# Optimization experiments

Hardware: AMD Instinct MI355X
Metric: run time of the kernel (lower is better)

The kernel has to match this reference:

```python
import jax, jax.numpy as jnp
import numpy as np

C = 512
NUM_HEADS = 8
GROUPS = 32
EPS = 1e-5


def setup_inputs() -> dict:
    key = jax.random.key(0)
    ks = jax.random.split(key, 7)
    B, H, W = 8, 32, 32
    x = jax.random.normal(ks[0], (B, C, H, W), dtype=jnp.float32)
    gn_w = jnp.ones((C,), dtype=jnp.float32)
    gn_b = jnp.zeros((C,), dtype=jnp.float32)
    # 1x1 convs as dense matrices [out, in]
    qkv_w = jax.random.normal(ks[1], (3 * C, C), dtype=jnp.float32) * (1.0 / np.sqrt(C))
    qkv_b = jnp.zeros((3 * C,), dtype=jnp.float32)
    proj_w = jax.random.normal(ks[2], (C, C), dtype=jnp.float32) * (1.0 / np.sqrt(C))
    proj_b = jnp.zeros((C,), dtype=jnp.float32)
    return {"x": x, "gn_w": gn_w, "gn_b": gn_b, "qkv_w": qkv_w,
            "qkv_b": qkv_b, "proj_w": proj_w, "proj_b": proj_b}


def reference(x, gn_w, gn_b, qkv_w, qkv_b, proj_w, proj_b):
    B, Cc, H, W = x.shape
    nh = NUM_HEADS
    d = Cc // nh
    N = H * W

    # GroupNorm(32, C) with affine
    xg = x.reshape(B, GROUPS, Cc // GROUPS, H, W)
    mean = jnp.mean(xg, axis=(2, 3, 4), keepdims=True)
    var = jnp.var(xg, axis=(2, 3, 4), keepdims=True)
    hn = ((xg - mean) * jax.lax.rsqrt(var + EPS)).reshape(B, Cc, H, W)
    hn = hn * gn_w[None, :, None, None] + gn_b[None, :, None, None]

    # 1x1 conv QKV projection: [B, 3C, H, W]
    qkv = jnp.einsum('oc,bchw->bohw', qkv_w, hn) + qkv_b[None, :, None, None]
    q, k, v = jnp.split(qkv, 3, axis=1)

    def to_heads(t):  # [B, C, H, W] -> [B, nh, N, d]
        return t.reshape(B, nh, d, N).transpose(0, 1, 3, 2)

    q, k, v = to_heads(q), to_heads(k), to_heads(v)
    scale = d ** (-0.5)
    attn = jax.nn.softmax(jnp.einsum('bhnd,bhmd->bhnm', q, k) * scale, axis=-1)
    o = jnp.einsum('bhnm,bhmd->bhnd', attn, v)          # [B, nh, N, d]
    o = o.transpose(0, 1, 3, 2).reshape(B, Cc, H, W)

    # 1x1 conv output projection + residual
    o = jnp.einsum('oc,bchw->bohw', proj_w, o) + proj_b[None, :, None, None]
    return x + o
```

## Files before the change

### kernel.cpp

```cpp
#include <hip/hip_runtime.h>

typedef __bf16 bf16x8 __attribute__((ext_vector_type(8)));
typedef float f32x4 __attribute__((ext_vector_type(4)));

#define MFMA(a, b, c) __builtin_amdgcn_mfma_f32_16x16x32_bf16(a, b, c, 0, 0, 0)

#define CS 0.18033688011112042f

__device__ __forceinline__ ushort f2bf(float f) {
    __bf16 h = (__bf16)f;
    return *(ushort*)&h;
}

__device__ __forceinline__ void stage_tile64(ushort* lds, const ushort* gbase,
                                             int row_stride, int nchunks,
                                             int wave, int lane) {
    int r8 = lane >> 3;
    int cswz = ((lane & 7) ^ r8) << 4;
#pragma unroll
    for (int c = wave; c < nchunks; c += 4) {
        const char* g = (const char*)(gbase + (size_t)(c * 8 + r8) * row_stride) + cswz;
        __builtin_amdgcn_global_load_lds(
            (const __attribute__((address_space(1))) unsigned int*)g,
            (__attribute__((address_space(3))) unsigned int*)((char*)lds + c * 1024),
            16, 0, 0);
    }
}

__device__ __forceinline__ bf16x8 lds_read_row(const ushort* lds, int row, int cb) {
    return *(const bf16x8*)((const char*)lds + row * 128 + (cb ^ ((row & 7) << 4)));
}

__global__ __launch_bounds__(256) void gn_cvt_kernel(const float* __restrict__ x,
                                                     const float* __restrict__ gnw,
                                                     const float* __restrict__ gnb,
                                                     ushort* __restrict__ hnT,
                                                     const float* __restrict__ w1,
                                                     const float* __restrict__ w2,
                                                     ushort* __restrict__ o1,
                                                     ushort* __restrict__ o2) {
    if (blockIdx.x >= 256) {
        int t = (blockIdx.x - 256) * 256 + threadIdx.x;
        const int n1q = (1536 * 512) / 4;
        float4 v;
        ushort* dst;
        int idx;
        if (t < n1q) {
            v = ((const float4*)w1)[t]; dst = o1; idx = t;
        } else {
            idx = t - n1q;
            v = ((const float4*)w2)[idx]; dst = o2;
        }
        ushort4 p;
        p.x = f2bf(v.x); p.y = f2bf(v.y); p.z = f2bf(v.z); p.w = f2bf(v.w);
        ((ushort4*)dst)[idx] = p;
        return;
    }

    int b = blockIdx.x >> 5, g = blockIdx.x & 31;
    const float* xp = x + (size_t)(b * 512 + g * 16) * 1024;
    int t = threadIdx.x;

    float s = 0.f, ss = 0.f;
    const float4* xp4 = (const float4*)xp;
    for (int i = t; i < 4096; i += 256) {
        float4 v = xp4[i];
        s += (v.x + v.y) + (v.z + v.w);
        ss += (v.x * v.x + v.y * v.y) + (v.z * v.z + v.w * v.w);
    }
#pragma unroll
    for (int off = 32; off >= 1; off >>= 1) {
        s += __shfl_xor(s, off);
        ss += __shfl_xor(ss, off);
    }
    __shared__ float red[8];
    __shared__ float sw[16], sb[16];
    int wave = t >> 6;
    if ((t & 63) == 0) { red[wave] = s; red[wave + 4] = ss; }
    if (t < 16) { sw[t] = gnw[g * 16 + t]; sb[t] = gnb[g * 16 + t]; }
    __syncthreads();
    float S = red[0] + red[1] + red[2] + red[3];
    float SS = red[4] + red[5] + red[6] + red[7];
    float mean = S * (1.0f / 16384.0f);
    float var = SS * (1.0f / 16384.0f) - mean * mean;
    float rstd = rsqrtf(var + 1e-5f);

    __shared__ ushort tile[16][258];
    int cc0 = (t & 3) * 4;
    int nb = t >> 2;
    for (int chunk = 0; chunk < 4; ++chunk) {
        __syncthreads();
#pragma unroll
        for (int cc = 0; cc < 16; ++cc) {
            float v = xp[cc * 1024 + chunk * 256 + t];
            tile[cc][t] = f2bf((v - mean) * rstd * sw[cc] + sb[cc]);
        }
        __syncthreads();
        size_t rowbase = (size_t)b * 1024 + chunk * 256;
#pragma unroll
        for (int k = 0; k < 4; ++k) {
            int nl = nb + 64 * k;
            ushort4 p;
            p.x = tile[cc0 + 0][nl];
            p.y = tile[cc0 + 1][nl];
            p.z = tile[cc0 + 2][nl];
            p.w = tile[cc0 + 3][nl];
            *(ushort4*)(hnT + (rowbase + nl) * 512 + g * 16 + cc0) = p;
        }
    }
}

__global__ __launch_bounds__(256) void gemm_qkv(const ushort* __restrict__ Wb,
                                                const ushort* __restrict__ hnT,
                                                const float* __restrict__ qkvb,
                                                ushort* __restrict__ qT,
                                                ushort* __restrict__ kT,
                                                ushort* __restrict__ vb) {
    int lane = threadIdx.x & 63, wave = threadIdx.x >> 6;
    int l15 = lane & 15, lg = lane >> 4;
    int bi = blockIdx.x;
    int b = bi & 7;
    int slot = bi >> 3;
    int m0 = (slot % 12) * 128;
    int n0 = (slot / 12) * 128;
    int mw = (wave >> 1) * 64, nw = (wave & 1) * 64;
    const ushort* bb = hnT + (size_t)b * 524288;

    __shared__ ushort abuf[2][8192];
    __shared__ ushort bbuf[2][8192];

    f32x4 acc[4][4] = {};
    stage_tile64(abuf[0], Wb + (size_t)m0 * 512, 512, 16, wave, lane);
    stage_tile64(bbuf[0], bb + (size_t)n0 * 512, 512, 16, wave, lane);
    __syncthreads();
    int cur = 0;
#pragma unroll 1
    for (int t = 0; t < 8; ++t) {
        if (t < 7) {
            stage_tile64(abuf[cur ^ 1], Wb + (size_t)m0 * 512 + (t + 1) * 64, 512, 16, wave, lane);
            stage_tile64(bbuf[cur ^ 1], bb + (size_t)n0 * 512 + (t + 1) * 64, 512, 16, wave, lane);
        }
#pragma unroll
        for (int kh = 0; kh < 2; kh++) {
            bf16x8 af[4], bfr[4];
#pragma unroll
            for (int i = 0; i < 4; i++)
                af[i] = lds_read_row(abuf[cur], mw + i * 16 + l15, kh * 64 + lg * 16);
#pragma unroll
            for (int j = 0; j < 4; j++)
                bfr[j] = lds_read_row(bbuf[cur], nw + j * 16 + l15, kh * 64 + lg * 16);
#pragma unroll
            for (int i = 0; i < 4; i++)
#pragma unroll
                for (int j = 0; j < 4; j++)
                    acc[i][j] = MFMA(af[i], bfr[j], acc[i][j]);
        }
        __syncthreads();
        cur ^= 1;
    }

#pragma unroll
    for (int i = 0; i < 4; i++) {
        int ob = m0 + mw + i * 16 + lg * 4;
        float bias[4];
#pragma unroll
        for (int r = 0; r < 4; r++) bias[r] = qkvb[ob + r];
        int part = ob >> 9;
        int oo = ob & 511;
#pragma unroll
        for (int j = 0; j < 4; j++) {
            int n = n0 + nw + j * 16 + l15;
            if (part == 2) {
                int L = n & 63;
                int cf = L >> 4;
                int s = ((cf >> 1) << 5) | (((L >> 2) & 3) << 3) | ((cf & 1) << 2) | (L & 3);
                int np = (n & ~63) | s;
#pragma unroll
                for (int r = 0; r < 4; r++)
                    vb[(size_t)(b * 512 + oo + r) * 1024 + np] = f2bf(acc[i][j][r] + bias[r]);
            } else {
                ushort* dst = part ? kT : qT;
                float sc = part ? 1.0f : CS;
                int h = oo >> 6, dd = oo & 63;
                ushort4 p;
                p.x = f2bf((acc[i][j][0] + bias[0]) * sc);
                p.y = f2bf((acc[i][j][1] + bias[1]) * sc);
                p.z = f2bf((acc[i][j][2] + bias[2]) * sc);
                p.w = f2bf((acc[i][j][3] + bias[3]) * sc);
                *(ushort4*)(dst + ((size_t)((b * 8 + h) * 1024 + n)) * 64 + dd) = p;
            }
        }
    }
}

__global__ __launch_bounds__(256) void attn_kernel(const ushort* __restrict__ qT,
                                                   const ushort* __restrict__ kT,
                                                   const ushort* __restrict__ vb,
                                                   ushort* __restrict__ aoT) {
    int bi = blockIdx.x;
    int bh = ((bi >> 6) << 3) | (bi & 7);
    int q0 = ((bi >> 3) & 7) * 128;
    int b = bh >> 3, h = bh & 7;
    int lane = threadIdx.x & 63, wave = threadIdx.x >> 6;
    int l15 = lane & 15, lg = lane >> 4;
    const ushort* qp = qT + (size_t)bh * 65536;
    const ushort* kp = kT + (size_t)bh * 65536;
    const ushort* vp = vb + (size_t)bh * 65536;

    __shared__ ushort kbuf[3][4096];
    __shared__ ushort vbuf[3][4096];

    bf16x8 vone;
#pragma unroll
    for (int e = 0; e < 8; e++) vone[e] = (__bf16)1.0f;

    bf16x8 qf[2][2];
#pragma unroll
    for (int i = 0; i < 2; i++)
#pragma unroll
        for (int kh = 0; kh < 2; kh++)
            qf[i][kh] = *(const bf16x8*)(qp + (size_t)(q0 + wave * 32 + i * 16 + l15) * 64 + kh * 32 + lg * 8);

    f32x4 oacc[2][4] = {};
    f32x4 lacc[2] = {};

    stage_tile64(kbuf[0], kp, 64, 8, wave, lane);
    stage_tile64(vbuf[0], vp, 1024, 8, wave, lane);
    stage_tile64(kbuf[1], kp + 4096, 64, 8, wave, lane);
    stage_tile64(vbuf[1], vp + 64, 1024, 8, wave, lane);
    asm volatile("s_waitcnt vmcnt(4)" ::: "memory");
    __builtin_amdgcn_s_barrier();

    int cur = 0;
#pragma unroll 1
    for (int t = 0; t < 16; ++t) {
        if (t < 14) {
            int nxt = cur + 2; if (nxt >= 3) nxt -= 3;
            stage_tile64(kbuf[nxt], kp + (size_t)(t + 2) * 4096, 64, 8, wave, lane);
            stage_tile64(vbuf[nxt], vp + (t + 2) * 64, 1024, 8, wave, lane);
        }
        const ushort* kb = kbuf[cur];
        const ushort* vc = vbuf[cur];

        f32x4 sacc[2][4] = {};
        __builtin_amdgcn_s_setprio(1);
#pragma unroll
        for (int kh = 0; kh < 2; kh++)
#pragma unroll
            for (int cf = 0; cf < 4; cf++) {
                bf16x8 kf = lds_read_row(kb, cf * 16 + l15, kh * 64 + lg * 16);
                sacc[0][cf] = MFMA(kf, qf[0][kh], sacc[0][cf]);
                sacc[1][cf] = MFMA(kf, qf[1][kh], sacc[1][cf]);
            }
        __builtin_amdgcn_s_setprio(0);

        bf16x8 vf[2][4];
#pragma unroll
        for (int ks = 0; ks < 2; ks++)
#pragma unroll
            for (int cf = 0; cf < 4; cf++)
                vf[ks][cf] = lds_read_row(vc, cf * 16 + l15, ks * 64 + lg * 16);

        bf16x8 pa[2][2];
#pragma unroll
        for (int i = 0; i < 2; i++)
#pragma unroll
            for (int ks = 0; ks < 2; ks++) {
                bf16x8 tr;
#pragma unroll
                for (int jhi = 0; jhi < 2; jhi++)
#pragma unroll
                    for (int r = 0; r < 4; r++)
                        tr[jhi * 4 + r] = (__bf16)exp2f(sacc[i][ks * 2 + jhi][r]);
                pa[i][ks] = tr;
            }

        __builtin_amdgcn_s_setprio(1);
#pragma unroll
        for (int i = 0; i < 2; i++)
#pragma unroll
            for (int ks = 0; ks < 2; ks++) {
                lacc[i] = MFMA(pa[i][ks], vone, lacc[i]);
#pragma unroll
                for (int cf = 0; cf < 4; cf++)
                    oacc[i][cf] = MFMA(pa[i][ks], vf[ks][cf], oacc[i][cf]);
            }
        __builtin_amdgcn_s_setprio(0);

        if (t < 15) {
            if (t < 14) asm volatile("s_waitcnt vmcnt(4)" ::: "memory");
            else        asm volatile("s_waitcnt vmcnt(0)" ::: "memory");
            __builtin_amdgcn_s_barrier();
        }
        cur = cur + 1; if (cur == 3) cur = 0;
    }

#pragma unroll
    for (int i = 0; i < 2; i++)
#pragma unroll
        for (int r = 0; r < 4; r++) {
            float inv = 1.0f / lacc[i][r];
            int n = q0 + wave * 32 + i * 16 + lg * 4 + r;
            size_t obase = ((size_t)b * 1024 + n) * 512 + h * 64;
#pragma unroll
            for (int cf = 0; cf < 4; cf++)
                aoT[obase + cf * 16 + l15] = f2bf(oacc[i][cf][r] * inv);
        }
}

__global__ __launch_bounds__(256) void gemm_proj(const ushort* __restrict__ Wb,
                                                 const ushort* __restrict__ aoT,
                                                 const float* __restrict__ projb,
                                                 const float* __restrict__ x,
                                                 float* __restrict__ out) {
    int lane = threadIdx.x & 63, wave = threadIdx.x >> 6;
    int l15 = lane & 15, lg = lane >> 4;
    int bi = blockIdx.x;
    int b = bi & 7;
    int slot = bi >> 3;
    int m0 = (slot & 3) * 128;
    int n0 = (slot >> 2) * 64;
    int mw = (wave >> 1) * 64, nw = (wave & 1) * 32;
    const ushort* bb = aoT + (size_t)b * 524288;

    __shared__ ushort abuf[2][8192];
    __shared__ ushort bbuf[2][4096];

    f32x4 acc[4][2] = {};
    stage_tile64(abuf[0], Wb + (size_t)m0 * 512, 512, 16, wave, lane);
    stage_tile64(bbuf[0], bb + (size_t)n0 * 512, 512, 8, wave, lane);
    __syncthreads();
    int cur = 0;
#pragma unroll 1
    for (int t = 0; t < 8; ++t) {
        if (t < 7) {
            stage_tile64(abuf[cur ^ 1], Wb + (size_t)m0 * 512 + (t + 1) * 64, 512, 16, wave, lane);
            stage_tile64(bbuf[cur ^ 1], bb + (size_t)n0 * 512 + (t + 1) * 64, 512, 8, wave, lane);
        }
#pragma unroll
        for (int kh = 0; kh < 2; kh++) {
            bf16x8 af[4], bfr[2];
#pragma unroll
            for (int i = 0; i < 4; i++)
                af[i] = lds_read_row(abuf[cur], mw + i * 16 + l15, kh * 64 + lg * 16);
#pragma unroll
            for (int j = 0; j < 2; j++)
                bfr[j] = lds_read_row(bbuf[cur], nw + j * 16 + l15, kh * 64 + lg * 16);
#pragma unroll
            for (int i = 0; i < 4; i++)
#pragma unroll
                for (int j = 0; j < 2; j++)
                    acc[i][j] = MFMA(af[i], bfr[j], acc[i][j]);
        }
        __syncthreads();
        cur ^= 1;
    }

#pragma unroll
    for (int i = 0; i < 4; i++) {
        int ob = m0 + mw + i * 16 + lg * 4;
        float bias[4];
#pragma unroll
        for (int r = 0; r < 4; r++) bias[r] = projb[ob + r];
#pragma unroll
        for (int j = 0; j < 2; j++) {
            int n = n0 + nw + j * 16 + l15;
#pragma unroll
            for (int r = 0; r < 4; r++) {
                size_t idx = (size_t)(b * 512 + ob + r) * 1024 + n;
                out[idx] = x[idx] + bias[r] + acc[i][j][r];
            }
        }
    }
}

extern "C" void kernel_launch(void* const* d_in, const int* in_sizes, int n_in,
                              void* d_out, int out_size, void* d_ws, size_t ws_size,
                              hipStream_t stream) {
    const float* x     = (const float*)d_in[0];
    const float* gnw   = (const float*)d_in[1];
    const float* gnb   = (const float*)d_in[2];
    const float* qkvw  = (const float*)d_in[3];
    const float* qkvb  = (const float*)d_in[4];
    const float* projw = (const float*)d_in[5];
    const float* projb = (const float*)d_in[6];
    float* out = (float*)d_out;

    char* ws = (char*)d_ws;
    ushort* hnT    = (ushort*)(ws);
    ushort* qT     = (ushort*)(ws + (size_t)(8u << 20));
    ushort* kT     = (ushort*)(ws + (size_t)(16u << 20));
    ushort* vbuf   = (ushort*)(ws + (size_t)(24u << 20));
    ushort* qkvwb  = (ushort*)(ws + (size_t)(32u << 20));
    ushort* projwb = (ushort*)(ws + (size_t)(32u << 20) + 1572864);

    gn_cvt_kernel<<<dim3(1280), dim3(256), 0, stream>>>(x, gnw, gnb, hnT,
                                                        qkvw, projw, qkvwb, projwb);
    gemm_qkv<<<dim3(768), dim3(256), 0, stream>>>(qkvwb, hnT, qkvb, qT, kT, vbuf);
    attn_kernel<<<dim3(512), dim3(256), 0, stream>>>(qT, kT, vbuf, hnT );
    gemm_proj<<<dim3(512), dim3(256), 0, stream>>>(projwb, hnT, projb, x, out);
}
```

Baseline: 86.70 us.

## Deepen GEMM pipelines to 4-stage K=32 ring with explicit vmcnt waits

Both the QKV and output projection GEMMs now walk K in 32-wide steps through a 4-buffer LDS ring, keeping three tiles in flight instead of double-buffering 64-wide tiles. A new 64-byte-row swizzle is added for staging and LDS reads. Full __syncthreads are replaced with partial s_waitcnt vmcnt plus s_barrier, and MFMA sections are wrapped in s_setprio. The goal is to hide global-load latency behind compute, at the cost of twice as many barrier iterations and fragile hand-counted vmcnt values.

```diff
diff --git a/kernel.cpp b/kernel.cpp
--- a/kernel.cpp
+++ b/kernel.cpp
@@ -29,6 +29,25 @@
 
 __device__ __forceinline__ bf16x8 lds_read_row(const ushort* lds, int row, int cb) {
     return *(const bf16x8*)((const char*)lds + row * 128 + (cb ^ ((row & 7) << 4)));
+}
+
+__device__ __forceinline__ void stage_tile32(ushort* lds, const ushort* gbase,
+                                             int row_stride, int nchunks,
+                                             int wave, int lane) {
+    int r16 = lane >> 2;
+    int csw = (((lane & 3) ^ ((lane >> 3) & 3)) << 3);
+#pragma unroll
+    for (int c = wave; c < nchunks; c += 4) {
+        const ushort* g = gbase + (size_t)(c * 16 + r16) * row_stride + csw;
+        __builtin_amdgcn_global_load_lds(
+            (const __attribute__((address_space(1))) unsigned int*)g,
+            (__attribute__((address_space(3))) unsigned int*)((char*)lds + c * 1024),
+            16, 0, 0);
+    }
+}
+
+__device__ __forceinline__ bf16x8 lds_read_row32(const ushort* lds, int row, int cb) {
+    return *(const bf16x8*)((const char*)lds + row * 64 + (cb ^ (((row >> 1) & 3) << 4)));
 }
 
 __global__ __launch_bounds__(256) void gn_cvt_kernel(const float* __restrict__ x,
@@ -124,39 +143,50 @@
     int m0 = (slot % 12) * 128;
     int n0 = (slot / 12) * 128;
     int mw = (wave >> 1) * 64, nw = (wave & 1) * 64;
-    const ushort* bb = hnT + (size_t)b * 524288;
-
-    __shared__ ushort abuf[2][8192];
-    __shared__ ushort bbuf[2][8192];
+    const ushort* Ag = Wb + (size_t)m0 * 512;
+    const ushort* Bg = hnT + (size_t)b * 524288 + (size_t)n0 * 512;
+
+    __shared__ ushort abuf[4][4096];
+    __shared__ ushort bbuf[4][4096];
 
     f32x4 acc[4][4] = {};
-    stage_tile64(abuf[0], Wb + (size_t)m0 * 512, 512, 16, wave, lane);
-    stage_tile64(bbuf[0], bb + (size_t)n0 * 512, 512, 16, wave, lane);
-    __syncthreads();
-    int cur = 0;
+#pragma unroll
+    for (int p = 0; p < 3; ++p) {
+        stage_tile32(abuf[p], Ag + p * 32, 512, 8, wave, lane);
+        stage_tile32(bbuf[p], Bg + p * 32, 512, 8, wave, lane);
+    }
+    asm volatile("s_waitcnt vmcnt(8)" ::: "memory");
+    __builtin_amdgcn_s_barrier();
+
 #pragma unroll 1
-    for (int t = 0; t < 8; ++t) {
-        if (t < 7) {
-            stage_tile64(abuf[cur ^ 1], Wb + (size_t)m0 * 512 + (t + 1) * 64, 512, 16, wave, lane);
-            stage_tile64(bbuf[cur ^ 1], bb + (size_t)n0 * 512 + (t + 1) * 64, 512, 16, wave, lane);
-        }
-#pragma unroll
-        for (int kh = 0; kh < 2; kh++) {
-            bf16x8 af[4], bfr[4];
-#pragma unroll
-            for (int i = 0; i < 4; i++)
-                af[i] = lds_read_row(abuf[cur], mw + i * 16 + l15, kh * 64 + lg * 16);
+    for (int t = 0; t < 16; ++t) {
+        if (t < 13) {
+            int nxt = (t + 3) & 3;
+            stage_tile32(abuf[nxt], Ag + (t + 3) * 32, 512, 8, wave, lane);
+            stage_tile32(bbuf[nxt], Bg + (t + 3) * 32, 512, 8, wave, lane);
+        }
+        const ushort* A = abuf[t & 3];
+        const ushort* B = bbuf[t & 3];
+        bf16x8 af[4], bfr[4];
+#pragma unroll
+        for (int i = 0; i < 4; i++)
+            af[i] = lds_read_row32(A, mw + i * 16 + l15, lg * 16);
+#pragma unroll
+        for (int j = 0; j < 4; j++)
+            bfr[j] = lds_read_row32(B, nw + j * 16 + l15, lg * 16);
+        __builtin_amdgcn_s_setprio(1);
+#pragma unroll
+        for (int i = 0; i < 4; i++)
 #pragma unroll
             for (int j = 0; j < 4; j++)
-                bfr[j] = lds_read_row(bbuf[cur], nw + j * 16 + l15, kh * 64 + lg * 16);
-#pragma unroll
-            for (int i = 0; i < 4; i++)
-#pragma unroll
-                for (int j = 0; j < 4; j++)
-                    acc[i][j] = MFMA(af[i], bfr[j], acc[i][j]);
-        }
-        __syncthreads();
-        cur ^= 1;
+                acc[i][j] = MFMA(af[i], bfr[j], acc[i][j]);
+        __builtin_amdgcn_s_setprio(0);
+        if (t < 15) {
+            if (t < 13)      asm volatile("s_waitcnt vmcnt(8)" ::: "memory");
+            else if (t == 13) asm volatile("s_waitcnt vmcnt(4)" ::: "memory");
+            else              asm volatile("s_waitcnt vmcnt(0)" ::: "memory");
+            __builtin_amdgcn_s_barrier();
+        }
     }
 
 #pragma unroll
@@ -321,39 +351,50 @@
     int m0 = (slot & 3) * 128;
     int n0 = (slot >> 2) * 64;
     int mw = (wave >> 1) * 64, nw = (wave & 1) * 32;
-    const ushort* bb = aoT + (size_t)b * 524288;
-
-    __shared__ ushort abuf[2][8192];
-    __shared__ ushort bbuf[2][4096];
+    const ushort* Ag = Wb + (size_t)m0 * 512;
+    const ushort* Bg = aoT + (size_t)b * 524288 + (size_t)n0 * 512;
+
+    __shared__ ushort abuf[4][4096];
+    __shared__ ushort bbuf[4][2048];
 
     f32x4 acc[4][2] = {};
-    stage_tile64(abuf[0], Wb + (size_t)m0 * 512, 512, 16, wave, lane);
-    stage_tile64(bbuf[0], bb + (size_t)n0 * 512, 512, 8, wave, lane);
-    __syncthreads();
-    int cur = 0;
+#pragma unroll
+    for (int p = 0; p < 3; ++p) {
+        stage_tile32(abuf[p], Ag + p * 32, 512, 8, wave, lane);
+        stage_tile32(bbuf[p], Bg + p * 32, 512, 4, wave, lane);
+    }
+    asm volatile("s_waitcnt vmcnt(6)" ::: "memory");
+    __builtin_amdgcn_s_barrier();
+
 #pragma unroll 1
-    for (int t = 0; t < 8; ++t) {
-        if (t < 7) {
-            stage_tile64(abuf[cur ^ 1], Wb + (size_t)m0 * 512 + (t + 1) * 64, 512, 16, wave, lane);
-            stage_tile64(bbuf[cur ^ 1], bb + (size_t)n0 * 512 + (t + 1) * 64, 512, 8, wave, lane);
-        }
-#pragma unroll
-        for (int kh = 0; kh < 2; kh++) {
-            bf16x8 af[4], bfr[2];
-#pragma unroll
-            for (int i = 0; i < 4; i++)
-                af[i] = lds_read_row(abuf[cur], mw + i * 16 + l15, kh * 64 + lg * 16);
+    for (int t = 0; t < 16; ++t) {
+        if (t < 13) {
+            int nxt = (t + 3) & 3;
+            stage_tile32(abuf[nxt], Ag + (t + 3) * 32, 512, 8, wave, lane);
+            stage_tile32(bbuf[nxt], Bg + (t + 3) * 32, 512, 4, wave, lane);
+        }
+        const ushort* A = abuf[t & 3];
+        const ushort* B = bbuf[t & 3];
+        bf16x8 af[4], bfr[2];
+#pragma unroll
+        for (int i = 0; i < 4; i++)
+            af[i] = lds_read_row32(A, mw + i * 16 + l15, lg * 16);
+#pragma unroll
+        for (int j = 0; j < 2; j++)
+            bfr[j] = lds_read_row32(B, nw + j * 16 + l15, lg * 16);
+        __builtin_amdgcn_s_setprio(1);
+#pragma unroll
+        for (int i = 0; i < 4; i++)
 #pragma unroll
             for (int j = 0; j < 2; j++)
-                bfr[j] = lds_read_row(bbuf[cur], nw + j * 16 + l15, kh * 64 + lg * 16);
-#pragma unroll
-            for (int i = 0; i < 4; i++)
-#pragma unroll
-                for (int j = 0; j < 2; j++)
-                    acc[i][j] = MFMA(af[i], bfr[j], acc[i][j]);
-        }
-        __syncthreads();
-        cur ^= 1;
+                acc[i][j] = MFMA(af[i], bfr[j], acc[i][j]);
+        __builtin_amdgcn_s_setprio(0);
+        if (t < 15) {
+            if (t < 13)      asm volatile("s_waitcnt vmcnt(6)" ::: "memory");
+            else if (t == 13) asm volatile("s_waitcnt vmcnt(3)" ::: "memory");
+            else              asm volatile("s_waitcnt vmcnt(0)" ::: "memory");
+            __builtin_amdgcn_s_barrier();
+        }
     }
 
 #pragma unroll
```

Measured after the change: 86.38 us. Within noise of the previous version (-0.4%).
